# Kernel tuning notes

Measured on AMD Instinct MI355X. Metric: run time of the kernel, lower is better.

The kernel has to match this reference:

```python
import jax, jax.numpy as jnp
import numpy as np

EPS = 1e-8

def _fft_unit_proj(x):
    # Project each vector to unit magnitude in the Fourier domain (norm_kv=True).
    f = jnp.fft.fft(x, axis=-1)
    return jnp.real(jnp.fft.ifft(f / (jnp.abs(f) + EPS), axis=-1))

def _hrr_key_value_query(k, v, q, causal=True):
    # k, v, q: [B, S, D]
    k = _fft_unit_proj(k)
    v = _fft_unit_proj(v)
    # bind: circular convolution of key and value
    kv = jnp.real(jnp.fft.ifft(jnp.fft.fft(k, axis=-1) * jnp.fft.fft(v, axis=-1), axis=-1))
    # causal associative memory: running sum of bound pairs along sequence
    if causal:
        mem = jnp.cumsum(kv, axis=1)
    else:
        mem = jnp.broadcast_to(jnp.sum(kv, axis=1, keepdims=True), kv.shape)
    # unbind: circular correlation of memory with query
    out = jnp.real(jnp.fft.ifft(jnp.conj(jnp.fft.fft(q, axis=-1)) * jnp.fft.fft(mem, axis=-1), axis=-1))
    return out


def setup_inputs() -> dict:
    key = jax.random.key(0)
    ks = jax.random.split(key, 8)
    B, S, D = 2, 4096, 2048
    sc = 1.0 / np.sqrt(D).astype(np.float32)
    return {
        "hidden_states": jax.random.normal(ks[0], (B, S, D), jnp.float32),
        "base_output": jax.random.normal(ks[1], (B, S, D), jnp.float32),
        "Wq": jax.random.normal(ks[2], (D, D), jnp.float32) * sc,
        "bq": jnp.zeros((D,), jnp.float32),
        "Wk": jax.random.normal(ks[3], (D, D), jnp.float32) * sc,
        "bk": jnp.zeros((D,), jnp.float32),
        "Wv": jax.random.normal(ks[4], (D, D), jnp.float32) * sc,
        "bv": jnp.zeros((D,), jnp.float32),
        "gate": jax.random.normal(ks[5], (1,), jnp.float32) * 0.1,
    }


def reference(hidden_states, base_output, Wq, bq, Wk, bk, Wv, bv, gate):
    # Adapter q/k/v projections (nn.Linear uses y = x @ W.T + b)
    q = jnp.einsum('bsd,ed->bse', hidden_states, Wq) + bq
    k = jnp.einsum('bsd,ed->bse', hidden_states, Wk) + bk
    v = jnp.einsum('bsd,ed->bse', hidden_states, Wv) + bv
    adapter = _hrr_key_value_query(k, v, q, causal=True)
    return base_output + gate * adapter
```

## Files before the change

kernel.cpp:

```cpp
#include <hip/hip_runtime.h>
#include <math.h>

constexpr int D_DIM  = 2048;
constexpr int HALF_D = 1024;
constexpr int B_DIM  = 2;
constexpr int S_DIM  = 4096;
constexpr int NROW   = B_DIM * S_DIM;
constexpr int NCHUNK = 64;
constexpr int CHLEN  = S_DIM / NCHUNK;
constexpr float EPS_ = 1e-8f;

typedef __attribute__((ext_vector_type(8))) short  short8;
typedef __attribute__((ext_vector_type(8))) unsigned short ushort8;
typedef __attribute__((ext_vector_type(4))) float  f32x4;

__device__ __forceinline__ float2 mkf2(float x, float y){ float2 r; r.x=x; r.y=y; return r; }
__device__ __forceinline__ float2 cmulf(float2 a, float2 b){
  return mkf2(fmaf(a.x, b.x, -a.y*b.y), fmaf(a.x, b.y, a.y*b.x));
}
__device__ __forceinline__ unsigned short f2bf(float x){
  unsigned u = __float_as_uint(x);
  u += 0x7fff + ((u >> 16) & 1);
  return (unsigned short)(u >> 16);
}
__device__ __forceinline__ float bf2f(unsigned short h){
  return __uint_as_float(((unsigned)h) << 16);
}

__global__ __launch_bounds__(256)
void cvt_inputs(const float* __restrict__ hs, const float* __restrict__ Wq,
                const float* __restrict__ Wk, const float* __restrict__ Wv,
                unsigned short* __restrict__ hsb, unsigned short* __restrict__ wb)
{
  constexpr int n8 = (NROW * D_DIM) / 8;
  constexpr int w8 = (D_DIM * D_DIM) / 8;
  int i = blockIdx.x * 256 + threadIdx.x;
  const float* src;
  unsigned short* dst;
  int local;
  if (i < n8) { src = hs; local = i; dst = hsb + (size_t)i * 8; }
  else {
    int j = i - n8;
    int seg = j >> 19;
    local = j & (w8 - 1);
    src = (seg == 0) ? Wq : (seg == 1) ? Wk : Wv;
    dst = wb + (size_t)j * 8;
  }
  const float4* p = (const float4*)src + (size_t)local * 2;
  float4 a = p[0], b = p[1];
  ushort8 o;
  o[0]=f2bf(a.x); o[1]=f2bf(a.y); o[2]=f2bf(a.z); o[3]=f2bf(a.w);
  o[4]=f2bf(b.x); o[5]=f2bf(b.y); o[6]=f2bf(b.z); o[7]=f2bf(b.w);
  *(ushort8*)dst = o;
}

__global__ __launch_bounds__(512, 2)
void gemm_fused(const unsigned short* __restrict__ A,
                const unsigned short* __restrict__ Wc,
                const float* __restrict__ bq, const float* __restrict__ bk,
                const float* __restrict__ bv,
                unsigned short* __restrict__ qb, unsigned short* __restrict__ kvb)
{
  constexpr int K = 2048, NITER = 16;
  __shared__ unsigned short lds[65536];
  const int tid  = threadIdx.x;
  const int wid  = tid >> 6, lane = tid & 63;
  const int wr   = wid >> 2, wc = wid & 3;

  int bid = blockIdx.x;
  int sw  = (bid & 7) * 96 + (bid >> 3);
  const int bm = (sw / 24) * 256, bn = (sw % 24) * 256;

  const int srow = tid >> 3;
  const int skc  = ((tid & 7) ^ (srow & 7)) * 8;
  const unsigned short* Ag = A  + (size_t)(bm + srow) * K + skc;
  const unsigned short* Bg = Wc + (size_t)(bn + srow) * K + skc;
  unsigned short* Al = lds;
  unsigned short* Bl = lds + 32768;
  const int stoff = wid * 512;

  auto stA = [&](int kt, int d, int h, int r) {
    __builtin_amdgcn_global_load_lds(
      (const __attribute__((address_space(1))) void*)(Ag + (size_t)(h * 128 + r * 64) * K + kt * 64),
      (__attribute__((address_space(3))) void*)(Al + d * 16384 + h * 8192 + r * 4096 + stoff),
      16, 0, 0);
  };
  auto stB = [&](int kt, int d, int h, int r) {
    __builtin_amdgcn_global_load_lds(
      (const __attribute__((address_space(1))) void*)(Bg + (size_t)(h * 128 + r * 64) * K + kt * 64),
      (__attribute__((address_space(3))) void*)(Bl + d * 16384 + h * 8192 + r * 4096 + stoff),
      16, 0, 0);
  };

  const int frow = lane & 15;
  const int kq   = lane >> 4;
  int ksw[2];
  ksw[0] = ((0 * 4 + kq) ^ (frow & 7)) * 8;
  ksw[1] = ((1 * 4 + kq) ^ (frow & 7)) * 8;
  const int arow0 = (wr * 128 + frow) * 64;
  const int brow0 = (wc * 64 + frow) * 64;

  f32x4 acc[8][4];
#pragma unroll
  for (int i = 0; i < 8; ++i)
#pragma unroll
    for (int j = 0; j < 4; ++j) acc[i][j] = (f32x4){0.f, 0.f, 0.f, 0.f};

  stA(0, 0, 0, 0); stA(0, 0, 0, 1); stA(0, 0, 1, 0); stA(0, 0, 1, 1);
  stB(0, 0, 0, 0); stB(0, 0, 0, 1); stB(0, 0, 1, 0); stB(0, 0, 1, 1);
  stB(1, 1, 0, 0); stB(1, 1, 0, 1); stB(1, 1, 1, 0); stB(1, 1, 1, 1);
  asm volatile("s_waitcnt vmcnt(4)" ::: "memory");
  __builtin_amdgcn_s_barrier();
  __builtin_amdgcn_sched_barrier(0);

#pragma unroll 1
  for (int it = 0; it < NITER; ++it) {
    const bool nl = (it < NITER - 1);
    const int t1 = 2 * it + 1;
    short8 bfr[8];
#pragma unroll
    for (int ph = 0; ph < 8; ++ph) {
      const int g  = ph & 3;
      const int db = ph >> 2;
      const unsigned short* Ab = Al + db * 16384;
      const unsigned short* Bb = Bl + db * 16384;

      if      (ph == 0) { stA(t1, 1, 0, 0); stA(t1, 1, 0, 1); }
      else if (ph == 1) { stA(t1, 1, 1, 0); stA(t1, 1, 1, 1); }
      else if (ph == 2) { if (nl) { stB(t1 + 1, 0, 0, 0); stB(t1 + 1, 0, 0, 1); } }
      else if (ph == 3) { if (nl) { stB(t1 + 1, 0, 1, 0); stB(t1 + 1, 0, 1, 1); } }
      else if (ph == 4) { if (nl) { stA(t1 + 1, 0, 0, 0); stA(t1 + 1, 0, 0, 1); } }
      else if (ph == 5) { if (nl) { stA(t1 + 1, 0, 1, 0); stA(t1 + 1, 0, 1, 1); } }
      else if (ph == 6) { if (nl) { stB(t1 + 2, 1, 0, 0); stB(t1 + 2, 1, 0, 1); } }
      else              { if (nl) { stB(t1 + 2, 1, 1, 0); stB(t1 + 2, 1, 1, 1); } }

      short8 af[2][2];
#pragma unroll
      for (int q = 0; q < 2; ++q)
#pragma unroll
        for (int ks = 0; ks < 2; ++ks)
          af[q][ks] = *(const short8*)(Ab + arow0 + (2 * g + q) * 1024 + ksw[ks]);
      if (g == 0) {
#pragma unroll
        for (int nf = 0; nf < 4; ++nf)
#pragma unroll
          for (int ks = 0; ks < 2; ++ks)
            bfr[nf * 2 + ks] = *(const short8*)(Bb + brow0 + nf * 1024 + ksw[ks]);
      }

      __builtin_amdgcn_s_barrier();
      asm volatile("s_waitcnt lgkmcnt(0)" ::: "memory");
      __builtin_amdgcn_sched_barrier(0);
      __builtin_amdgcn_s_setprio(1);
#pragma unroll
      for (int ks = 0; ks < 2; ++ks)
#pragma unroll
        for (int q = 0; q < 2; ++q)
#pragma unroll
          for (int nf = 0; nf < 4; ++nf)
            acc[2 * g + q][nf] = __builtin_amdgcn_mfma_f32_16x16x32_bf16(
                af[q][ks], bfr[nf * 2 + ks], acc[2 * g + q][nf], 0, 0, 0);
      __builtin_amdgcn_s_setprio(0);

      if (ph == 3) {
        if (nl) asm volatile("s_waitcnt vmcnt(4)" ::: "memory");
        else    asm volatile("s_waitcnt vmcnt(0)" ::: "memory");
      } else if (ph == 7) {
        if (nl) asm volatile("s_waitcnt vmcnt(4)" ::: "memory");
      }
      __builtin_amdgcn_s_barrier();
    }
  }

  const int seg = bn >> 11;
  const float* bp = (seg == 0) ? bq : (seg == 1) ? bk : bv;
  float bias_j[4];
#pragma unroll
  for (int j = 0; j < 4; ++j)
    bias_j[j] = bp[(bn + wc * 64 + j * 16 + frow) & 2047];
  const int er = (lane >> 4) * 4;
  unsigned short* dst = (seg == 0) ? qb : kvb;
  const size_t rstride = (seg == 0) ? 2048 : 4096;
  const int coff = (seg == 2) ? 2048 : 0;
#pragma unroll
  for (int I = 0; I < 8; ++I) {
    int row = bm + wr * 128 + I * 16 + er;
#pragma unroll
    for (int j = 0; j < 4; ++j) {
      int col = (bn + wc * 64 + j * 16 + frow) & 2047;
#pragma unroll
      for (int r = 0; r < 4; ++r) {
        float val = acc[I][j][r] + bias_j[j];
        dst[(size_t)(row + r) * rstride + coff + col] = f2bf(val);
      }
    }
  }
}

__device__ __forceinline__ int XS(int i){ return i ^ (((i >> 5) ^ (i >> 10)) & 31); }
__device__ __forceinline__ int TS(int i){ return i ^ ((i >> 5) & 31); }

__device__ __forceinline__ float2 mulmi(float2 w){ return mkf2(w.y, -w.x); }
__device__ __forceinline__ float2 mulw8(float2 w){
  const float c = 0.70710678118654752f;
  return mkf2(c * (w.x + w.y), c * (w.y - w.x));
}
__device__ __forceinline__ void bfly(float2& a, float2& b, float2 w){
  float2 v = cmulf(w, b);
  b = mkf2(a.x - v.x, a.y - v.y);
  a = mkf2(a.x + v.x, a.y + v.y);
}
__device__ __forceinline__ void bflyc(float2& a, float2& b, float2 w){
  float2 d = mkf2(a.x - b.x, a.y - b.y);
  a = mkf2(a.x + b.x, a.y + b.y);
  b = mkf2(fmaf(d.x, w.x, d.y * w.y), fmaf(d.y, w.x, -d.x * w.y));
}

__device__ __forceinline__ void fwd8(float2 e[8], float2 wA, float2 wB0, float2 wC0){
  bfly(e[0], e[1], wA); bfly(e[2], e[3], wA); bfly(e[4], e[5], wA); bfly(e[6], e[7], wA);
  float2 wB1 = mulmi(wB0);
  bfly(e[0], e[2], wB0); bfly(e[1], e[3], wB1); bfly(e[4], e[6], wB0); bfly(e[5], e[7], wB1);
  float2 wC1 = mulw8(wC0), wC2 = mulmi(wC0), wC3 = mulmi(wC1);
  bfly(e[0], e[4], wC0); bfly(e[1], e[5], wC1); bfly(e[2], e[6], wC2); bfly(e[3], e[7], wC3);
}
__device__ __forceinline__ void inv8(float2 e[8], float2 wA, float2 wB0, float2 wC0){
  float2 wC1 = mulw8(wC0), wC2 = mulmi(wC0), wC3 = mulmi(wC1);
  bflyc(e[0], e[4], wC0); bflyc(e[1], e[5], wC1); bflyc(e[2], e[6], wC2); bflyc(e[3], e[7], wC3);
  float2 wB1 = mulmi(wB0);
  bflyc(e[0], e[2], wB0); bflyc(e[1], e[3], wB1); bflyc(e[4], e[6], wB0); bflyc(e[5], e[7], wB1);
  bflyc(e[0], e[1], wA); bflyc(e[2], e[3], wA); bflyc(e[4], e[5], wA); bflyc(e[6], e[7], wA);
}

__device__ __forceinline__ float2 twld(const float* twr, const float* twi, int i){
  int s = TS(i);
  return mkf2(twr[s], twi[s]);
}

__device__ void fft_fwd(float2* X, const float* twr, const float* twi, int t)
{
  const float2 one = mkf2(1.f, 0.f);
  {
    int b = 8 * t;
    float2 e[8];
#pragma unroll
    for (int r = 0; r < 8; ++r) e[r] = X[XS(b + r)];
    fwd8(e, one, one, one);
#pragma unroll
    for (int r = 0; r < 8; ++r) X[XS(b + r)] = e[r];
  }
  __syncthreads();
  {
    int u = t >> 5, b = 64 * (t & 31) + u;
    float2 e[8];
#pragma unroll
    for (int r = 0; r < 8; ++r) e[r] = X[XS(b + 8 * r)];
    fwd8(e, twld(twr,twi,128*u), twld(twr,twi,64*u), twld(twr,twi,32*u));
#pragma unroll
    for (int r = 0; r < 8; ++r) X[XS(b + 8 * r)] = e[r];
  }
  __syncthreads();
  {
    int u = t & 63, b = 512 * (t >> 6) + u;
    float2 e[8];
#pragma unroll
    for (int r = 0; r < 8; ++r) e[r] = X[XS(b + 64 * r)];
    fwd8(e, twld(twr,twi,16*u), twld(twr,twi,8*u), twld(twr,twi,4*u));
#pragma unroll
    for (int r = 0; r < 8; ++r) X[XS(b + 64 * r)] = e[r];
  }
  __syncthreads();
#pragma unroll
  for (int h = 0; h < 2; ++h) {
    int u = t + 256 * h;
    float2 f[4];
#pragma unroll
    for (int r = 0; r < 4; ++r) f[r] = X[XS(u + 512 * r)];
    float2 wA = twld(twr,twi,2*u), wB0 = twld(twr,twi,u), wB1 = mulmi(wB0);
    bfly(f[0], f[1], wA);  bfly(f[2], f[3], wA);
    bfly(f[0], f[2], wB0); bfly(f[1], f[3], wB1);
#pragma unroll
    for (int r = 0; r < 4; ++r) X[XS(u + 512 * r)] = f[r];
  }
  __syncthreads();
}

__device__ void fft_inv(float2* X, const float* twr, const float* twi, int t)
{
  const float2 one = mkf2(1.f, 0.f);
#pragma unroll
  for (int h = 0; h < 2; ++h) {
    int u = t + 256 * h;
    float2 f[4];
#pragma unroll
    for (int r = 0; r < 4; ++r) f[r] = X[XS(u + 512 * r)];
    float2 wA = twld(twr,twi,2*u), wB0 = twld(twr,twi,u), wB1 = mulmi(wB0);
    bflyc(f[0], f[2], wB0); bflyc(f[1], f[3], wB1);
    bflyc(f[0], f[1], wA);  bflyc(f[2], f[3], wA);
#pragma unroll
    for (int r = 0; r < 4; ++r) X[XS(u + 512 * r)] = f[r];
  }
  __syncthreads();
  {
    int u = t & 63, b = 512 * (t >> 6) + u;
    float2 e[8];
#pragma unroll
    for (int r = 0; r < 8; ++r) e[r] = X[XS(b + 64 * r)];
    inv8(e, twld(twr,twi,16*u), twld(twr,twi,8*u), twld(twr,twi,4*u));
#pragma unroll
    for (int r = 0; r < 8; ++r) X[XS(b + 64 * r)] = e[r];
  }
  __syncthreads();
  {
    int u = t >> 5, b = 64 * (t & 31) + u;
    float2 e[8];
#pragma unroll
    for (int r = 0; r < 8; ++r) e[r] = X[XS(b + 8 * r)];
    inv8(e, twld(twr,twi,128*u), twld(twr,twi,64*u), twld(twr,twi,32*u));
#pragma unroll
    for (int r = 0; r < 8; ++r) X[XS(b + 8 * r)] = e[r];
  }
  __syncthreads();
  {
    int b = 8 * t;
    float2 e[8];
#pragma unroll
    for (int r = 0; r < 8; ++r) e[r] = X[XS(b + r)];
    inv8(e, one, one, one);
#pragma unroll
    for (int r = 0; r < 8; ++r) X[XS(b + r)] = e[r];
  }
  __syncthreads();
}

__global__ __launch_bounds__(256)
void twiddle_init(float2* __restrict__ twg)
{
  int i = blockIdx.x * 256 + threadIdx.x;
  if (i < HALF_D) {
    float sv, cv;
    sincosf(-6.283185307179586f * (float)i / (float)D_DIM, &sv, &cv);
    twg[i] = mkf2(cv, sv);
  }
}

__global__ __launch_bounds__(256)
void fftkv_kernel(unsigned short* __restrict__ kvb, const float2* __restrict__ twg)
{
  __shared__ float2 X[D_DIM];
  __shared__ float twr[HALF_D], twi[HALF_D];
  const int t = threadIdx.x;
  const size_t row = blockIdx.x;
  const unsigned short* kvrow = kvb + row * 4096;

  for (int i = t; i < HALF_D; i += 256) {
    float2 w = twg[i]; int s = TS(i); twr[s] = w.x; twi[s] = w.y;
  }
  {
    int i0 = t * 8;
    ushort8 k8 = *(const ushort8*)(kvrow + i0);
    ushort8 v8 = *(const ushort8*)(kvrow + 2048 + i0);
#pragma unroll
    for (int r = 0; r < 8; ++r) {
      int i = i0 + r;
      int p = __brev((unsigned)i) >> 21;
      X[XS(p)] = mkf2(bf2f(k8[r]), bf2f(v8[r]));
    }
  }
  __syncthreads();
  fft_fwd(X, twr, twi, t);

  unsigned int* outp = (unsigned int*)(kvb + row * 4096);
  for (int d = t; d < HALF_D; d += 256) {
    float2 p;
    if (d == 0) {
      float2 z0 = X[XS(0)], zn = X[XS(HALF_D)];
      float k0 = z0.x, v0 = z0.y, kn = zn.x, vn = zn.y;
      float p0 = (k0 / (fabsf(k0) + EPS_)) * (v0 / (fabsf(v0) + EPS_));
      float pn = (kn / (fabsf(kn) + EPS_)) * (vn / (fabsf(vn) + EPS_));
      p = mkf2(p0, pn);
    } else {
      float2 A = X[XS(d)];
      float2 Bc = X[XS(D_DIM - d)];
      float2 Bj = mkf2(Bc.x, -Bc.y);
      float2 Fk = mkf2(0.5f * (A.x + Bj.x), 0.5f * (A.y + Bj.y));
      float2 tt = mkf2(0.5f * (A.x - Bj.x), 0.5f * (A.y - Bj.y));
      float2 Fv = mkf2(tt.y, -tt.x);
      float sa = 1.f / (sqrtf(Fk.x*Fk.x + Fk.y*Fk.y) + EPS_);
      float sb = 1.f / (sqrtf(Fv.x*Fv.x + Fv.y*Fv.y) + EPS_);
      p = cmulf(Fk, Fv);
      float sc = sa * sb;
      p.x *= sc; p.y *= sc;
    }
    outp[d] = (unsigned)f2bf(p.x) | ((unsigned)f2bf(p.y) << 16);
  }
}

__global__ __launch_bounds__(256)
void scan_partial(const unsigned short* __restrict__ kvb, float2* __restrict__ part)
{
  int gid = blockIdx.x * 256 + threadIdx.x;
  int q4 = gid & 255;
  int chunk = (gid >> 8) & (NCHUNK - 1);
  int b = gid >> 14;
  const unsigned short* p = kvb + (size_t)(b * S_DIM + chunk * CHLEN) * 4096 + q4 * 8;
  float ar[4] = {0,0,0,0}, ai[4] = {0,0,0,0};
  for (int s = 0; s < CHLEN; ++s) {
    ushort8 v = *(const ushort8*)(p + (size_t)s * 4096);
#pragma unroll
    for (int e = 0; e < 4; ++e) { ar[e] += bf2f(v[2*e]); ai[e] += bf2f(v[2*e+1]); }
  }
  float2* pp = part + (size_t)(b * NCHUNK + chunk) * HALF_D + q4 * 4;
#pragma unroll
  for (int e = 0; e < 4; ++e) pp[e] = mkf2(ar[e], ai[e]);
}

__global__ __launch_bounds__(256)
void scan_apply(unsigned short* __restrict__ kvb, const float2* __restrict__ part)
{
  int gid = blockIdx.x * 256 + threadIdx.x;
  int q4 = gid & 255;
  int chunk = (gid >> 8) & (NCHUNK - 1);
  int b = gid >> 14;
  unsigned short* p = kvb + (size_t)(b * S_DIM + chunk * CHLEN) * 4096 + q4 * 8;
  const float2* pb = part + (size_t)b * (NCHUNK * HALF_D) + q4 * 4;
  float ar[4] = {0.f,0.f,0.f,0.f}, ai[4] = {0.f,0.f,0.f,0.f};
  for (int c = 0; c < chunk; ++c) {
    const float2* pp = pb + (size_t)c * HALF_D;
#pragma unroll
    for (int e = 0; e < 4; ++e) { float2 v = pp[e]; ar[e] += v.x; ai[e] += v.y; }
  }
  for (int s = 0; s < CHLEN; ++s) {
    ushort8 v = *(const ushort8*)(p + (size_t)s * 4096);
    ushort8 o;
#pragma unroll
    for (int e = 0; e < 4; ++e) {
      ar[e] += bf2f(v[2*e]); ai[e] += bf2f(v[2*e+1]);
      o[2*e] = f2bf(ar[e]); o[2*e+1] = f2bf(ai[e]);
    }
    *(ushort8*)(p + (size_t)s * 4096) = o;
  }
}

__global__ __launch_bounds__(256)
void final_kernel(const unsigned short* __restrict__ qb,
                  const unsigned short* __restrict__ kvb,
                  const float* __restrict__ base, const float* __restrict__ gate,
                  const float2* __restrict__ twg, float* __restrict__ out)
{
  __shared__ float2 X[D_DIM];
  __shared__ float twr[HALF_D], twi[HALF_D];
  const int t = threadIdx.x;
  const size_t row0 = (size_t)blockIdx.x * 2;
  const unsigned short* qrow = qb + row0 * 2048;
  const unsigned short* m0 = kvb + row0 * 4096;
  const unsigned short* m1 = m0 + 4096;

  for (int i = t; i < HALF_D; i += 256) {
    float2 w = twg[i]; int s = TS(i); twr[s] = w.x; twi[s] = w.y;
  }
  {
    int i0 = t * 8;
    ushort8 q0 = *(const ushort8*)(qrow + i0);
    ushort8 q1 = *(const ushort8*)(qrow + 2048 + i0);
#pragma unroll
    for (int r = 0; r < 8; ++r) {
      int i = i0 + r;
      int p = __brev((unsigned)i) >> 21;
      X[XS(p)] = mkf2(bf2f(q0[r]), bf2f(q1[r]));
    }
  }
  __syncthreads();
  fft_fwd(X, twr, twi, t);

  for (int d = t; d < HALF_D; d += 256) {
    if (d == 0) {
      float2 z0 = X[XS(0)], zn = X[XS(HALF_D)];
      float M00 = bf2f(m0[0]), M0N = bf2f(m0[1]);
      float M10 = bf2f(m1[0]), M1N = bf2f(m1[1]);
      X[XS(0)]      = mkf2(z0.x * M00, z0.y * M10);
      X[XS(HALF_D)] = mkf2(zn.x * M0N, zn.y * M1N);
    } else {
      float2 Zd = X[XS(d)];
      float2 Zn = X[XS(D_DIM - d)];
      float2 Fq0 = mkf2(0.5f * (Zd.x + Zn.x), 0.5f * (Zd.y - Zn.y));
      float2 td  = mkf2(0.5f * (Zd.x - Zn.x), 0.5f * (Zd.y + Zn.y));
      float2 Fq1 = mkf2(td.y, -td.x);
      float2 M0d = mkf2(bf2f(m0[2*d]), bf2f(m0[2*d+1]));
      float2 M1d = mkf2(bf2f(m1[2*d]), bf2f(m1[2*d+1]));
      float2 G0 = mkf2(Fq0.x*M0d.x + Fq0.y*M0d.y, Fq0.x*M0d.y - Fq0.y*M0d.x);
      float2 G1 = mkf2(Fq1.x*M1d.x + Fq1.y*M1d.y, Fq1.x*M1d.y - Fq1.y*M1d.x);
      X[XS(d)]         = mkf2(G0.x - G1.y, G0.y + G1.x);
      X[XS(D_DIM - d)] = mkf2(G0.x + G1.y, G1.x - G0.y);
    }
  }
  __syncthreads();
  fft_inv(X, twr, twi, t);

  const float gv = gate[0] * (1.f / (float)D_DIM);
  const float* brow = base + row0 * 2048;
  float* orow = out + row0 * 2048;
  for (int i = t; i < D_DIM; i += 256) {
    int p = __brev((unsigned)i) >> 21;
    float2 y = X[XS(p)];
    orow[i]        = brow[i]        + gv * y.x;
    orow[2048 + i] = brow[2048 + i] + gv * y.y;
  }
}

extern "C" void kernel_launch(void* const* d_in, const int* in_sizes, int n_in,
                              void* d_out, int out_size, void* d_ws, size_t ws_size,
                              hipStream_t stream)
{
  const float* hs   = (const float*)d_in[0];
  const float* base = (const float*)d_in[1];
  const float* Wq   = (const float*)d_in[2];
  const float* bq   = (const float*)d_in[3];
  const float* Wk   = (const float*)d_in[4];
  const float* bk   = (const float*)d_in[5];
  const float* Wv   = (const float*)d_in[6];
  const float* bv   = (const float*)d_in[7];
  const float* gate = (const float*)d_in[8];
  float* out  = (float*)d_out;

  char* ws = (char*)d_ws;
  unsigned short* hsb = (unsigned short*)ws;
  unsigned short* wqb = (unsigned short*)(ws + 33554432);
  unsigned short* kvb = (unsigned short*)(ws + 58720256);
  unsigned short* qb  = (unsigned short*)(ws + 58720256 + 67108864);
  float2* part = (float2*)(ws + 58720256 + 67108864 + 33554432);
  float2* twg  = (float2*)ws;

  {
    constexpr int n8 = (NROW * D_DIM) / 8;
    constexpr int w8 = (D_DIM * D_DIM) / 8;
    cvt_inputs<<<(n8 + 3 * w8) / 256, 256, 0, stream>>>(hs, Wq, Wk, Wv, hsb, wqb);
  }

  gemm_fused<<<768, 512, 0, stream>>>(hsb, wqb, bq, bk, bv, qb, kvb);

  twiddle_init<<<4, 256, 0, stream>>>(twg);

  fftkv_kernel<<<NROW, 256, 0, stream>>>(kvb, twg);

  scan_partial<<<128, 256, 0, stream>>>(kvb, part);
  scan_apply<<<128, 256, 0, stream>>>(kvb, part);

  final_kernel<<<NROW / 2, 256, 0, stream>>>(qb, kvb, base, gate, twg, out);
}
```

Baseline: 359.9 us.

## Fold DFT into projection weights so GEMM emits q/k/v spectra directly

Because the DFT is linear, the weight matrices and biases are transformed into the half-spectrum packed layout once per call. The GEMM then writes frequency-domain q, k and v straight away. This removes the per-row forward FFT of k/v and of q in the later kernels, leaving only an elementwise normalize-and-bind pass and the final inverse FFT. It adds a per-call weight FFT kernel with strided column reads of the fp32 weights. The q spectrum is now kept in bf16 rather than computed in fp32 inside the final kernel, which may cost some accuracy.

New measurement: 370.8 us. +3.0%, slower.

```diff
diff --git a/kernel.cpp b/kernel.cpp
--- a/kernel.cpp
+++ b/kernel.cpp
@@ -26,39 +26,232 @@
 __device__ __forceinline__ float bf2f(unsigned short h){
   return __uint_as_float(((unsigned)h) << 16);
 }
-
-__global__ __launch_bounds__(256)
-void cvt_inputs(const float* __restrict__ hs, const float* __restrict__ Wq,
-                const float* __restrict__ Wk, const float* __restrict__ Wv,
-                unsigned short* __restrict__ hsb, unsigned short* __restrict__ wb)
-{
-  constexpr int n8 = (NROW * D_DIM) / 8;
-  constexpr int w8 = (D_DIM * D_DIM) / 8;
+__device__ __forceinline__ unsigned packbf2(float a, float b){
+  return (unsigned)f2bf(a) | ((unsigned)f2bf(b) << 16);
+}
+
+__global__ __launch_bounds__(256)
+void cvt_hs(const float* __restrict__ hs, unsigned short* __restrict__ hsb)
+{
   int i = blockIdx.x * 256 + threadIdx.x;
-  const float* src;
-  unsigned short* dst;
-  int local;
-  if (i < n8) { src = hs; local = i; dst = hsb + (size_t)i * 8; }
-  else {
-    int j = i - n8;
-    int seg = j >> 19;
-    local = j & (w8 - 1);
-    src = (seg == 0) ? Wq : (seg == 1) ? Wk : Wv;
-    dst = wb + (size_t)j * 8;
-  }
-  const float4* p = (const float4*)src + (size_t)local * 2;
+  const float4* p = (const float4*)hs + (size_t)i * 2;
   float4 a = p[0], b = p[1];
   ushort8 o;
   o[0]=f2bf(a.x); o[1]=f2bf(a.y); o[2]=f2bf(a.z); o[3]=f2bf(a.w);
   o[4]=f2bf(b.x); o[5]=f2bf(b.y); o[6]=f2bf(b.z); o[7]=f2bf(b.w);
-  *(ushort8*)dst = o;
+  *(ushort8*)(hsb + (size_t)i * 8) = o;
+}
+
+__device__ __forceinline__ int XS(int i){ return i ^ (((i >> 5) ^ (i >> 10)) & 31); }
+__device__ __forceinline__ int TS(int i){ return i ^ ((i >> 5) & 31); }
+
+__device__ __forceinline__ float2 mulmi(float2 w){ return mkf2(w.y, -w.x); }
+__device__ __forceinline__ float2 mulw8(float2 w){
+  const float c = 0.70710678118654752f;
+  return mkf2(c * (w.x + w.y), c * (w.y - w.x));
+}
+__device__ __forceinline__ void bfly(float2& a, float2& b, float2 w){
+  float2 v = cmulf(w, b);
+  b = mkf2(a.x - v.x, a.y - v.y);
+  a = mkf2(a.x + v.x, a.y + v.y);
+}
+__device__ __forceinline__ void bflyc(float2& a, float2& b, float2 w){
+  float2 d = mkf2(a.x - b.x, a.y - b.y);
+  a = mkf2(a.x + b.x, a.y + b.y);
+  b = mkf2(fmaf(d.x, w.x, d.y * w.y), fmaf(d.y, w.x, -d.x * w.y));
+}
+
+__device__ __forceinline__ void fwd8(float2 e[8], float2 wA, float2 wB0, float2 wC0){
+  bfly(e[0], e[1], wA); bfly(e[2], e[3], wA); bfly(e[4], e[5], wA); bfly(e[6], e[7], wA);
+  float2 wB1 = mulmi(wB0);
+  bfly(e[0], e[2], wB0); bfly(e[1], e[3], wB1); bfly(e[4], e[6], wB0); bfly(e[5], e[7], wB1);
+  float2 wC1 = mulw8(wC0), wC2 = mulmi(wC0), wC3 = mulmi(wC1);
+  bfly(e[0], e[4], wC0); bfly(e[1], e[5], wC1); bfly(e[2], e[6], wC2); bfly(e[3], e[7], wC3);
+}
+__device__ __forceinline__ void inv8(float2 e[8], float2 wA, float2 wB0, float2 wC0){
+  float2 wC1 = mulw8(wC0), wC2 = mulmi(wC0), wC3 = mulmi(wC1);
+  bflyc(e[0], e[4], wC0); bflyc(e[1], e[5], wC1); bflyc(e[2], e[6], wC2); bflyc(e[3], e[7], wC3);
+  float2 wB1 = mulmi(wB0);
+  bflyc(e[0], e[2], wB0); bflyc(e[1], e[3], wB1); bflyc(e[4], e[6], wB0); bflyc(e[5], e[7], wB1);
+  bflyc(e[0], e[1], wA); bflyc(e[2], e[3], wA); bflyc(e[4], e[5], wA); bflyc(e[6], e[7], wA);
+}
+
+__device__ __forceinline__ float2 twld(const float* twr, const float* twi, int i){
+  int s = TS(i);
+  return mkf2(twr[s], twi[s]);
+}
+
+__device__ __forceinline__ void load_twiddles_ls(float* twr, float* twi, int t)
+{
+  for (int i = t; i < HALF_D; i += 256) {
+    float sv, cv;
+    sincosf(-6.283185307179586f * (float)i / (float)D_DIM, &sv, &cv);
+    int s = TS(i); twr[s] = cv; twi[s] = sv;
+  }
+}
+
+__device__ void fft_fwd(float2* X, const float* twr, const float* twi, int t)
+{
+  const float2 one = mkf2(1.f, 0.f);
+  {
+    int b = 8 * t;
+    float2 e[8];
+#pragma unroll
+    for (int r = 0; r < 8; ++r) e[r] = X[XS(b + r)];
+    fwd8(e, one, one, one);
+#pragma unroll
+    for (int r = 0; r < 8; ++r) X[XS(b + r)] = e[r];
+  }
+  __syncthreads();
+  {
+    int u = t >> 5, b = 64 * (t & 31) + u;
+    float2 e[8];
+#pragma unroll
+    for (int r = 0; r < 8; ++r) e[r] = X[XS(b + 8 * r)];
+    fwd8(e, twld(twr,twi,128*u), twld(twr,twi,64*u), twld(twr,twi,32*u));
+#pragma unroll
+    for (int r = 0; r < 8; ++r) X[XS(b + 8 * r)] = e[r];
+  }
+  __syncthreads();
+  {
+    int u = t & 63, b = 512 * (t >> 6) + u;
+    float2 e[8];
+#pragma unroll
+    for (int r = 0; r < 8; ++r) e[r] = X[XS(b + 64 * r)];
+    fwd8(e, twld(twr,twi,16*u), twld(twr,twi,8*u), twld(twr,twi,4*u));
+#pragma unroll
+    for (int r = 0; r < 8; ++r) X[XS(b + 64 * r)] = e[r];
+  }
+  __syncthreads();
+#pragma unroll
+  for (int h = 0; h < 2; ++h) {
+    int u = t + 256 * h;
+    float2 f[4];
+#pragma unroll
+    for (int r = 0; r < 4; ++r) f[r] = X[XS(u + 512 * r)];
+    float2 wA = twld(twr,twi,2*u), wB0 = twld(twr,twi,u), wB1 = mulmi(wB0);
+    bfly(f[0], f[1], wA);  bfly(f[2], f[3], wA);
+    bfly(f[0], f[2], wB0); bfly(f[1], f[3], wB1);
+#pragma unroll
+    for (int r = 0; r < 4; ++r) X[XS(u + 512 * r)] = f[r];
+  }
+  __syncthreads();
+}
+
+__device__ void fft_inv(float2* X, const float* twr, const float* twi, int t)
+{
+  const float2 one = mkf2(1.f, 0.f);
+#pragma unroll
+  for (int h = 0; h < 2; ++h) {
+    int u = t + 256 * h;
+    float2 f[4];
+#pragma unroll
+    for (int r = 0; r < 4; ++r) f[r] = X[XS(u + 512 * r)];
+    float2 wA = twld(twr,twi,2*u), wB0 = twld(twr,twi,u), wB1 = mulmi(wB0);
+    bflyc(f[0], f[2], wB0); bflyc(f[1], f[3], wB1);
+    bflyc(f[0], f[1], wA);  bflyc(f[2], f[3], wA);
+#pragma unroll
+    for (int r = 0; r < 4; ++r) X[XS(u + 512 * r)] = f[r];
+  }
+  __syncthreads();
+  {
+    int u = t & 63, b = 512 * (t >> 6) + u;
+    float2 e[8];
+#pragma unroll
+    for (int r = 0; r < 8; ++r) e[r] = X[XS(b + 64 * r)];
+    inv8(e, twld(twr,twi,16*u), twld(twr,twi,8*u), twld(twr,twi,4*u));
+#pragma unroll
+    for (int r = 0; r < 8; ++r) X[XS(b + 64 * r)] = e[r];
+  }
+  __syncthreads();
+  {
+    int u = t >> 5, b = 64 * (t & 31) + u;
+    float2 e[8];
+#pragma unroll
+    for (int r = 0; r < 8; ++r) e[r] = X[XS(b + 8 * r)];
+    inv8(e, twld(twr,twi,128*u), twld(twr,twi,64*u), twld(twr,twi,32*u));
+#pragma unroll
+    for (int r = 0; r < 8; ++r) X[XS(b + 8 * r)] = e[r];
+  }
+  __syncthreads();
+  {
+    int b = 8 * t;
+    float2 e[8];
+#pragma unroll
+    for (int r = 0; r < 8; ++r) e[r] = X[XS(b + r)];
+    inv8(e, one, one, one);
+#pragma unroll
+    for (int r = 0; r < 8; ++r) X[XS(b + r)] = e[r];
+  }
+  __syncthreads();
+}
+
+__global__ __launch_bounds__(256)
+void wfft_kernel(const float* __restrict__ Wq, const float* __restrict__ Wk,
+                 const float* __restrict__ Wv, unsigned short* __restrict__ wspec)
+{
+  __shared__ float2 X[D_DIM];
+  __shared__ float twr[HALF_D], twi[HALF_D];
+  const int t = threadIdx.x;
+  const int b = blockIdx.x;
+  const int w = b >> 10, j = b & 1023;
+  const int d0 = (j & 7) * 256 + (j >> 3) * 2;
+  const float* Ws = (w == 0) ? Wq : (w == 1) ? Wk : Wv;
+
+  load_twiddles_ls(twr, twi, t);
+  for (int e = t; e < D_DIM; e += 256) {
+    int p = __brev((unsigned)e) >> 21;
+    float2 v = *(const float2*)(Ws + (size_t)e * 2048 + d0);
+    X[XS(p)] = v;
+  }
+  __syncthreads();
+  fft_fwd(X, twr, twi, t);
+
+  unsigned short* w0 = wspec + ((size_t)w * 2048) * 2048 + d0;
+  for (int d = t; d < HALF_D; d += 256) {
+    if (d == 0) {
+      float2 z0 = X[XS(0)], zn = X[XS(HALF_D)];
+      *(unsigned*)(w0)        = packbf2(z0.x, z0.y);
+      *(unsigned*)(w0 + 2048) = packbf2(zn.x, zn.y);
+    } else {
+      float2 A = X[XS(d)], Bc = X[XS(D_DIM - d)];
+      float2 Bj = mkf2(Bc.x, -Bc.y);
+      float2 F0 = mkf2(0.5f * (A.x + Bj.x), 0.5f * (A.y + Bj.y));
+      float2 tt = mkf2(0.5f * (A.x - Bj.x), 0.5f * (A.y - Bj.y));
+      float2 F1 = mkf2(tt.y, -tt.x);
+      *(unsigned*)(w0 + (size_t)(2 * d) * 2048)     = packbf2(F0.x, F1.x);
+      *(unsigned*)(w0 + (size_t)(2 * d + 1) * 2048) = packbf2(F0.y, F1.y);
+    }
+  }
+}
+
+__global__ __launch_bounds__(256)
+void biasfft_kernel(const float* __restrict__ bq, const float* __restrict__ bk,
+                    const float* __restrict__ bv, float* __restrict__ biasF)
+{
+  __shared__ float2 X[D_DIM];
+  __shared__ float twr[HALF_D], twi[HALF_D];
+  const int t = threadIdx.x;
+  const int w = blockIdx.x;
+  const float* bs = (w == 0) ? bq : (w == 1) ? bk : bv;
+  load_twiddles_ls(twr, twi, t);
+  for (int e = t; e < D_DIM; e += 256) {
+    int p = __brev((unsigned)e) >> 21;
+    X[XS(p)] = mkf2(bs[e], 0.f);
+  }
+  __syncthreads();
+  fft_fwd(X, twr, twi, t);
+  float* o = biasF + (size_t)w * 2048;
+  for (int d = t; d < HALF_D; d += 256) {
+    if (d == 0) { o[0] = X[XS(0)].x; o[1] = X[XS(HALF_D)].x; }
+    else { float2 z = X[XS(d)]; o[2*d] = z.x; o[2*d+1] = z.y; }
+  }
 }
 
 __global__ __launch_bounds__(512, 2)
 void gemm_fused(const unsigned short* __restrict__ A,
                 const unsigned short* __restrict__ Wc,
-                const float* __restrict__ bq, const float* __restrict__ bk,
-                const float* __restrict__ bv,
+                const float* __restrict__ biasF,
                 unsigned short* __restrict__ qb, unsigned short* __restrict__ kvb)
 {
   constexpr int K = 2048, NITER = 16;
@@ -173,7 +366,7 @@
   }
 
   const int seg = bn >> 11;
-  const float* bp = (seg == 0) ? bq : (seg == 1) ? bk : bv;
+  const float* bp = biasF + (size_t)seg * 2048;
   float bias_j[4];
 #pragma unroll
   for (int j = 0; j < 4; ++j)
@@ -197,202 +390,34 @@
   }
 }
 
-__device__ __forceinline__ int XS(int i){ return i ^ (((i >> 5) ^ (i >> 10)) & 31); }
-__device__ __forceinline__ int TS(int i){ return i ^ ((i >> 5) & 31); }
-
-__device__ __forceinline__ float2 mulmi(float2 w){ return mkf2(w.y, -w.x); }
-__device__ __forceinline__ float2 mulw8(float2 w){
-  const float c = 0.70710678118654752f;
-  return mkf2(c * (w.x + w.y), c * (w.y - w.x));
-}
-__device__ __forceinline__ void bfly(float2& a, float2& b, float2 w){
-  float2 v = cmulf(w, b);
-  b = mkf2(a.x - v.x, a.y - v.y);
-  a = mkf2(a.x + v.x, a.y + v.y);
-}
-__device__ __forceinline__ void bflyc(float2& a, float2& b, float2 w){
-  float2 d = mkf2(a.x - b.x, a.y - b.y);
-  a = mkf2(a.x + b.x, a.y + b.y);
-  b = mkf2(fmaf(d.x, w.x, d.y * w.y), fmaf(d.y, w.x, -d.x * w.y));
-}
-
-__device__ __forceinline__ void fwd8(float2 e[8], float2 wA, float2 wB0, float2 wC0){
-  bfly(e[0], e[1], wA); bfly(e[2], e[3], wA); bfly(e[4], e[5], wA); bfly(e[6], e[7], wA);
-  float2 wB1 = mulmi(wB0);
-  bfly(e[0], e[2], wB0); bfly(e[1], e[3], wB1); bfly(e[4], e[6], wB0); bfly(e[5], e[7], wB1);
-  float2 wC1 = mulw8(wC0), wC2 = mulmi(wC0), wC3 = mulmi(wC1);
-  bfly(e[0], e[4], wC0); bfly(e[1], e[5], wC1); bfly(e[2], e[6], wC2); bfly(e[3], e[7], wC3);
-}
-__device__ __forceinline__ void inv8(float2 e[8], float2 wA, float2 wB0, float2 wC0){
-  float2 wC1 = mulw8(wC0), wC2 = mulmi(wC0), wC3 = mulmi(wC1);
-  bflyc(e[0], e[4], wC0); bflyc(e[1], e[5], wC1); bflyc(e[2], e[6], wC2); bflyc(e[3], e[7], wC3);
-  float2 wB1 = mulmi(wB0);
-  bflyc(e[0], e[2], wB0); bflyc(e[1], e[3], wB1); bflyc(e[4], e[6], wB0); bflyc(e[5], e[7], wB1);
-  bflyc(e[0], e[1], wA); bflyc(e[2], e[3], wA); bflyc(e[4], e[5], wA); bflyc(e[6], e[7], wA);
-}
-
-__device__ __forceinline__ float2 twld(const float* twr, const float* twi, int i){
-  int s = TS(i);
-  return mkf2(twr[s], twi[s]);
-}
-
-__device__ void fft_fwd(float2* X, const float* twr, const float* twi, int t)
-{
-  const float2 one = mkf2(1.f, 0.f);
-  {
-    int b = 8 * t;
-    float2 e[8];
-#pragma unroll
-    for (int r = 0; r < 8; ++r) e[r] = X[XS(b + r)];
-    fwd8(e, one, one, one);
-#pragma unroll
-    for (int r = 0; r < 8; ++r) X[XS(b + r)] = e[r];
-  }
-  __syncthreads();
-  {
-    int u = t >> 5, b = 64 * (t & 31) + u;
-    float2 e[8];
-#pragma unroll
-    for (int r = 0; r < 8; ++r) e[r] = X[XS(b + 8 * r)];
-    fwd8(e, twld(twr,twi,128*u), twld(twr,twi,64*u), twld(twr,twi,32*u));
-#pragma unroll
-    for (int r = 0; r < 8; ++r) X[XS(b + 8 * r)] = e[r];
-  }
-  __syncthreads();
-  {
-    int u = t & 63, b = 512 * (t >> 6) + u;
-    float2 e[8];
-#pragma unroll
-    for (int r = 0; r < 8; ++r) e[r] = X[XS(b + 64 * r)];
-    fwd8(e, twld(twr,twi,16*u), twld(twr,twi,8*u), twld(twr,twi,4*u));
-#pragma unroll
-    for (int r = 0; r < 8; ++r) X[XS(b + 64 * r)] = e[r];
-  }
-  __syncthreads();
-#pragma unroll
-  for (int h = 0; h < 2; ++h) {
-    int u = t + 256 * h;
-    float2 f[4];
-#pragma unroll
-    for (int r = 0; r < 4; ++r) f[r] = X[XS(u + 512 * r)];
-    float2 wA = twld(twr,twi,2*u), wB0 = twld(twr,twi,u), wB1 = mulmi(wB0);
-    bfly(f[0], f[1], wA);  bfly(f[2], f[3], wA);
-    bfly(f[0], f[2], wB0); bfly(f[1], f[3], wB1);
-#pragma unroll
-    for (int r = 0; r < 4; ++r) X[XS(u + 512 * r)] = f[r];
-  }
-  __syncthreads();
-}
-
-__device__ void fft_inv(float2* X, const float* twr, const float* twi, int t)
-{
-  const float2 one = mkf2(1.f, 0.f);
-#pragma unroll
-  for (int h = 0; h < 2; ++h) {
-    int u = t + 256 * h;
-    float2 f[4];
-#pragma unroll
-    for (int r = 0; r < 4; ++r) f[r] = X[XS(u + 512 * r)];
-    float2 wA = twld(twr,twi,2*u), wB0 = twld(twr,twi,u), wB1 = mulmi(wB0);
-    bflyc(f[0], f[2], wB0); bflyc(f[1], f[3], wB1);
-    bflyc(f[0], f[1], wA);  bflyc(f[2], f[3], wA);
-#pragma unroll
-    for (int r = 0; r < 4; ++r) X[XS(u + 512 * r)] = f[r];
-  }
-  __syncthreads();
-  {
-    int u = t & 63, b = 512 * (t >> 6) + u;
-    float2 e[8];
-#pragma unroll
-    for (int r = 0; r < 8; ++r) e[r] = X[XS(b + 64 * r)];
-    inv8(e, twld(twr,twi,16*u), twld(twr,twi,8*u), twld(twr,twi,4*u));
-#pragma unroll
-    for (int r = 0; r < 8; ++r) X[XS(b + 64 * r)] = e[r];
-  }
-  __syncthreads();
-  {
-    int u = t >> 5, b = 64 * (t & 31) + u;
-    float2 e[8];
-#pragma unroll
-    for (int r = 0; r < 8; ++r) e[r] = X[XS(b + 8 * r)];
-    inv8(e, twld(twr,twi,128*u), twld(twr,twi,64*u), twld(twr,twi,32*u));
-#pragma unroll
-    for (int r = 0; r < 8; ++r) X[XS(b + 8 * r)] = e[r];
-  }
-  __syncthreads();
-  {
-    int b = 8 * t;
-    float2 e[8];
-#pragma unroll
-    for (int r = 0; r < 8; ++r) e[r] = X[XS(b + r)];
-    inv8(e, one, one, one);
-#pragma unroll
-    for (int r = 0; r < 8; ++r) X[XS(b + r)] = e[r];
-  }
-  __syncthreads();
-}
-
-__global__ __launch_bounds__(256)
-void twiddle_init(float2* __restrict__ twg)
-{
-  int i = blockIdx.x * 256 + threadIdx.x;
-  if (i < HALF_D) {
-    float sv, cv;
-    sincosf(-6.283185307179586f * (float)i / (float)D_DIM, &sv, &cv);
-    twg[i] = mkf2(cv, sv);
-  }
-}
-
-__global__ __launch_bounds__(256)
-void fftkv_kernel(unsigned short* __restrict__ kvb, const float2* __restrict__ twg)
-{
-  __shared__ float2 X[D_DIM];
-  __shared__ float twr[HALF_D], twi[HALF_D];
+__global__ __launch_bounds__(256)
+void normmul_kernel(unsigned short* __restrict__ kvb)
+{
+  const size_t row = blockIdx.x;
   const int t = threadIdx.x;
-  const size_t row = blockIdx.x;
-  const unsigned short* kvrow = kvb + row * 4096;
-
-  for (int i = t; i < HALF_D; i += 256) {
-    float2 w = twg[i]; int s = TS(i); twr[s] = w.x; twi[s] = w.y;
-  }
-  {
-    int i0 = t * 8;
-    ushort8 k8 = *(const ushort8*)(kvrow + i0);
-    ushort8 v8 = *(const ushort8*)(kvrow + 2048 + i0);
-#pragma unroll
-    for (int r = 0; r < 8; ++r) {
-      int i = i0 + r;
-      int p = __brev((unsigned)i) >> 21;
-      X[XS(p)] = mkf2(bf2f(k8[r]), bf2f(v8[r]));
-    }
-  }
-  __syncthreads();
-  fft_fwd(X, twr, twi, t);
-
-  unsigned int* outp = (unsigned int*)(kvb + row * 4096);
-  for (int d = t; d < HALF_D; d += 256) {
-    float2 p;
-    if (d == 0) {
-      float2 z0 = X[XS(0)], zn = X[XS(HALF_D)];
-      float k0 = z0.x, v0 = z0.y, kn = zn.x, vn = zn.y;
-      float p0 = (k0 / (fabsf(k0) + EPS_)) * (v0 / (fabsf(v0) + EPS_));
-      float pn = (kn / (fabsf(kn) + EPS_)) * (vn / (fabsf(vn) + EPS_));
-      p = mkf2(p0, pn);
+  unsigned short* kvrow = kvb + row * 4096;
+  ushort8 kk = *(const ushort8*)(kvrow + t * 8);
+  ushort8 vv = *(const ushort8*)(kvrow + 2048 + t * 8);
+  ushort8 o;
+#pragma unroll
+  for (int e = 0; e < 4; ++e) {
+    if (t == 0 && e == 0) {
+      float k0 = bf2f(kk[0]), kn = bf2f(kk[1]);
+      float v0 = bf2f(vv[0]), vn = bf2f(vv[1]);
+      o[0] = f2bf((k0 / (fabsf(k0) + EPS_)) * (v0 / (fabsf(v0) + EPS_)));
+      o[1] = f2bf((kn / (fabsf(kn) + EPS_)) * (vn / (fabsf(vn) + EPS_)));
     } else {
-      float2 A = X[XS(d)];
-      float2 Bc = X[XS(D_DIM - d)];
-      float2 Bj = mkf2(Bc.x, -Bc.y);
-      float2 Fk = mkf2(0.5f * (A.x + Bj.x), 0.5f * (A.y + Bj.y));
-      float2 tt = mkf2(0.5f * (A.x - Bj.x), 0.5f * (A.y - Bj.y));
-      float2 Fv = mkf2(tt.y, -tt.x);
+      float2 Fk = mkf2(bf2f(kk[2*e]), bf2f(kk[2*e+1]));
+      float2 Fv = mkf2(bf2f(vv[2*e]), bf2f(vv[2*e+1]));
       float sa = 1.f / (sqrtf(Fk.x*Fk.x + Fk.y*Fk.y) + EPS_);
       float sb = 1.f / (sqrtf(Fv.x*Fv.x + Fv.y*Fv.y) + EPS_);
-      p = cmulf(Fk, Fv);
+      float2 p = cmulf(Fk, Fv);
       float sc = sa * sb;
-      p.x *= sc; p.y *= sc;
+      o[2*e]   = f2bf(p.x * sc);
+      o[2*e+1] = f2bf(p.y * sc);
     }
-    outp[d] = (unsigned)f2bf(p.x) | ((unsigned)f2bf(p.y) << 16);
-  }
+  }
+  *(ushort8*)(kvrow + t * 8) = o;
 }
 
 __global__ __launch_bounds__(256)
@@ -445,46 +470,27 @@
 void final_kernel(const unsigned short* __restrict__ qb,
                   const unsigned short* __restrict__ kvb,
                   const float* __restrict__ base, const float* __restrict__ gate,
-                  const float2* __restrict__ twg, float* __restrict__ out)
+                  float* __restrict__ out)
 {
   __shared__ float2 X[D_DIM];
   __shared__ float twr[HALF_D], twi[HALF_D];
   const int t = threadIdx.x;
   const size_t row0 = (size_t)blockIdx.x * 2;
-  const unsigned short* qrow = qb + row0 * 2048;
+  const unsigned short* q0p = qb + row0 * 2048;
+  const unsigned short* q1p = q0p + 2048;
   const unsigned short* m0 = kvb + row0 * 4096;
   const unsigned short* m1 = m0 + 4096;
 
-  for (int i = t; i < HALF_D; i += 256) {
-    float2 w = twg[i]; int s = TS(i); twr[s] = w.x; twi[s] = w.y;
-  }
-  {
-    int i0 = t * 8;
-    ushort8 q0 = *(const ushort8*)(qrow + i0);
-    ushort8 q1 = *(const ushort8*)(qrow + 2048 + i0);
-#pragma unroll
-    for (int r = 0; r < 8; ++r) {
-      int i = i0 + r;
-      int p = __brev((unsigned)i) >> 21;
-      X[XS(p)] = mkf2(bf2f(q0[r]), bf2f(q1[r]));
-    }
-  }
-  __syncthreads();
-  fft_fwd(X, twr, twi, t);
-
+  load_twiddles_ls(twr, twi, t);
   for (int d = t; d < HALF_D; d += 256) {
     if (d == 0) {
-      float2 z0 = X[XS(0)], zn = X[XS(HALF_D)];
       float M00 = bf2f(m0[0]), M0N = bf2f(m0[1]);
       float M10 = bf2f(m1[0]), M1N = bf2f(m1[1]);
-      X[XS(0)]      = mkf2(z0.x * M00, z0.y * M10);
-      X[XS(HALF_D)] = mkf2(zn.x * M0N, zn.y * M1N);
+      X[XS(0)]      = mkf2(bf2f(q0p[0]) * M00, bf2f(q1p[0]) * M10);
+      X[XS(HALF_D)] = mkf2(bf2f(q0p[1]) * M0N, bf2f(q1p[1]) * M1N);
     } else {
-      float2 Zd = X[XS(d)];
-      float2 Zn = X[XS(D_DIM - d)];
-      float2 Fq0 = mkf2(0.5f * (Zd.x + Zn.x), 0.5f * (Zd.y - Zn.y));
-      float2 td  = mkf2(0.5f * (Zd.x - Zn.x), 0.5f * (Zd.y + Zn.y));
-      float2 Fq1 = mkf2(td.y, -td.x);
+      float2 Fq0 = mkf2(bf2f(q0p[2*d]), bf2f(q0p[2*d+1]));
+      float2 Fq1 = mkf2(bf2f(q1p[2*d]), bf2f(q1p[2*d+1]));
       float2 M0d = mkf2(bf2f(m0[2*d]), bf2f(m0[2*d+1]));
       float2 M1d = mkf2(bf2f(m1[2*d]), bf2f(m1[2*d+1]));
       float2 G0 = mkf2(Fq0.x*M0d.x + Fq0.y*M0d.y, Fq0.x*M0d.y - Fq0.y*M0d.x);
@@ -523,27 +529,23 @@
   float* out  = (float*)d_out;
 
   char* ws = (char*)d_ws;
-  unsigned short* hsb = (unsigned short*)ws;
-  unsigned short* wqb = (unsigned short*)(ws + 33554432);
-  unsigned short* kvb = (unsigned short*)(ws + 58720256);
-  unsigned short* qb  = (unsigned short*)(ws + 58720256 + 67108864);
-  float2* part = (float2*)(ws + 58720256 + 67108864 + 33554432);
-  float2* twg  = (float2*)ws;
-
-  {
-    constexpr int n8 = (NROW * D_DIM) / 8;
-    constexpr int w8 = (D_DIM * D_DIM) / 8;
-    cvt_inputs<<<(n8 + 3 * w8) / 256, 256, 0, stream>>>(hs, Wq, Wk, Wv, hsb, wqb);
-  }
-
-  gemm_fused<<<768, 512, 0, stream>>>(hsb, wqb, bq, bk, bv, qb, kvb);
-
-  twiddle_init<<<4, 256, 0, stream>>>(twg);
-
-  fftkv_kernel<<<NROW, 256, 0, stream>>>(kvb, twg);
+  unsigned short* hsb   = (unsigned short*)ws;
+  unsigned short* wspec = (unsigned short*)(ws + 33554432);
+  unsigned short* kvb   = (unsigned short*)(ws + 58720256);
+  unsigned short* qb    = (unsigned short*)(ws + 58720256 + 67108864);
+  float2* part  = (float2*)(ws + 58720256 + 67108864 + 33554432);
+  float*  biasF = (float*)part;
+
+  cvt_hs<<<8192, 256, 0, stream>>>(hs, hsb);
+  wfft_kernel<<<3072, 256, 0, stream>>>(Wq, Wk, Wv, wspec);
+  biasfft_kernel<<<3, 256, 0, stream>>>(bq, bk, bv, biasF);
+
+  gemm_fused<<<768, 512, 0, stream>>>(hsb, wspec, biasF, qb, kvb);
+
+  normmul_kernel<<<NROW, 256, 0, stream>>>(kvb);
 
   scan_partial<<<128, 256, 0, stream>>>(kvb, part);
   scan_apply<<<128, 256, 0, stream>>>(kvb, part);
 
-  final_kernel<<<NROW / 2, 256, 0, stream>>>(qb, kvb, base, gate, twg, out);
-}
+  final_kernel<<<NROW / 2, 256, 0, stream>>>(qb, kvb, base, gate, out);
+}
```
